# Kernel optimization log

Hardware: AMD Instinct MI355X
Metric: run time of the kernel (lower is better)

The kernel has to match this reference:

```python
import math
import jax, jax.numpy as jnp
import numpy as np

B, T, D = 4, 1024, 1024
H = 16
HD = D // H       # head_dim
DE = 64           # d_event
NT = 8            # n_event_types
NR = 64           # n_rules
NH = 4            # n_hits
NA = 2            # n_alternatives
SQ = math.sqrt(HD)


def setup_inputs() -> dict:
    key = jax.random.key(0)
    ks = jax.random.split(key, 16)
    s = 0.02
    f = jnp.float32
    return {
        "x": jax.random.normal(ks[0], (B, T, D), f),
        "W_node": jax.random.normal(ks[1], (D, D), f) * s,
        "W_value": jax.random.normal(ks[2], (D, D), f) * s,
        "W_out": jax.random.normal(ks[3], (D, D), f) * s,
        "arity_w": jax.random.normal(ks[4], (H, HD), f) * s,   # arity=3 -> one extra axis weight
        "W_event": jax.random.normal(ks[5], (D, DE), f) * s,
        "W_type": jax.random.normal(ks[6], (D, NT), f) * s,
        "patterns": jax.random.normal(ks[7], (NR, DE), f) * s,
        "W_actions": jax.random.normal(ks[8], (NA, D, D), f) * s,
        "W_alt": jax.random.normal(ks[9], (DE, NA), f) * s,
        "log_temp": jnp.zeros((), f),
        "Wg1": jax.random.normal(ks[10], (2 * D + 1, D), f) * s,
        "bg1": jnp.zeros((D,), f),
        "Wg2": jax.random.normal(ks[11], (D, 1), f) * s,
        "bg2": jnp.zeros((1,), f),
    }


def reference(x, W_node, W_value, W_out, arity_w, W_event, W_type, patterns,
              W_actions, W_alt, log_temp, Wg1, bg1, Wg2, bg2):
    # --- IsotropicAttention (arity=3, eval mode so dropout is identity) ---
    nodes = (x @ W_node).reshape(B, T, H, HD).transpose(0, 2, 1, 3)    # (B,H,T,HD)
    values = (x @ W_value).reshape(B, T, H, HD).transpose(0, 2, 1, 3)  # (B,H,T,HD)
    scores = jnp.einsum('bhtd,bhsd->bhts', nodes, nodes)
    scores = (scores + scores.transpose(0, 1, 3, 2)) * (0.5 / SQ)      # symmetrize + scale
    ax = jnp.einsum('bhtd,hd->bht', nodes, arity_w)                    # ternary axis score
    mod = jax.nn.sigmoid((ax[:, :, :, None] + ax[:, :, None, :]) / SQ)
    scores = scores * mod
    attn = jax.nn.softmax(scores, axis=-1)
    attn_out = jnp.einsum('bhts,bhsd->bthd', attn, values).reshape(B, T, D) @ W_out
    x1 = x + attn_out
    # --- EventGenerator ---
    events = x1 @ W_event                                              # (B,T,DE)
    event_types = jax.nn.softmax(x1 @ W_type, axis=-1)                 # (B,T,NT)
    # --- RuleBank: soft top-k hit activation ---
    en = events / jnp.maximum(jnp.linalg.norm(events, axis=-1, keepdims=True), 1e-12)
    pn = patterns / jnp.maximum(jnp.linalg.norm(patterns, axis=-1, keepdims=True), 1e-12)
    sim = en @ pn.T                                                    # (B,T,NR)
    topk_vals, topk_idx = jax.lax.top_k(sim, NH)
    temp = jnp.clip(jnp.exp(log_temp), 0.01, 10.0)
    hit_w = jax.nn.softmax(topk_vals / temp, axis=-1)                  # (B,T,NH)
    hit_patterns = patterns[topk_idx]                                  # (B,T,NH,DE)
    weighted_pattern = jnp.einsum('btkd,btk->btd', hit_patterns, hit_w)
    alt_w = jax.nn.softmax((weighted_pattern @ W_alt) / temp, axis=-1) # (B,T,NA)
    acted = jnp.einsum('btd,ade->btae', x1, W_actions)                 # (B,T,NA,D)
    actions_out = jnp.einsum('btae,bta->bte', acted, alt_w)
    hit_strength = jnp.max(topk_vals, axis=-1, keepdims=True)
    actions_out = actions_out * jax.nn.sigmoid(hit_strength)
    # --- TransactionGate: soft commit/rollback ---
    entropy = -jnp.sum(event_types * jnp.log(event_types + 1e-10), axis=-1, keepdims=True)
    entropy_norm = entropy / math.log(NT)
    gin = jnp.concatenate([x1, actions_out, entropy_norm], axis=-1)    # (B,T,2D+1)
    g = jax.nn.sigmoid(jax.nn.silu(gin @ Wg1 + bg1) @ Wg2 + bg2)       # (B,T,1)
    return x1 + g * actions_out
```

## Files before the change

kernel.cpp:

```cpp
#include <hip/hip_runtime.h>
#include <hip/hip_bf16.h>
#include <math.h>

#define B_  4
#define T_  1024
#define D_  1024
#define H_  16
#define HD_ 64
#define DE_ 64
#define NT_ 8
#define NR_ 64
#define NH_ 4

typedef __attribute__((ext_vector_type(8))) short short8;
typedef __attribute__((ext_vector_type(4))) short short4v;
typedef __attribute__((ext_vector_type(4))) float f4;

__device__ __forceinline__ short f2bf(float f) {
    unsigned x = __float_as_uint(f);
    unsigned r = (x + 0x7fffu + ((x >> 16) & 1u)) >> 16;
    return (short)r;
}
__device__ __forceinline__ float bf2f(short s) {
    return __uint_as_float(((unsigned)(unsigned short)s) << 16);
}

__global__ __launch_bounds__(256) void castx_k(
    const float* __restrict__ x, short* __restrict__ xb)
{
    size_t i = ((size_t)blockIdx.x * 256 + threadIdx.x) * 8;
    float4 v0 = *(const float4*)&x[i];
    float4 v1 = *(const float4*)&x[i + 4];
    short8 o;
    o[0] = f2bf(v0.x); o[1] = f2bf(v0.y); o[2] = f2bf(v0.z); o[3] = f2bf(v0.w);
    o[4] = f2bf(v1.x); o[5] = f2bf(v1.y); o[6] = f2bf(v1.z); o[7] = f2bf(v1.w);
    *(short8*)&xb[i] = o;
}

struct TJ { const float* src; short* dst; int K, N, rs, ro, base; };
struct TJobs { TJ j[7]; };

__global__ __launch_bounds__(256) void tcast_all(TJobs jb)
{
    int bid = blockIdx.x;
    int ji = 0;
#pragma unroll
    for (int i = 1; i < 7; i++) if (bid >= jb.j[i].base) ji = i;
    const float* src = jb.j[ji].src;
    short* dst = jb.j[ji].dst;
    const int K = jb.j[ji].K, N = jb.j[ji].N;
    const int rs = jb.j[ji].rs, ro = jb.j[ji].ro;
    int rel = bid - jb.j[ji].base;
    int tiles_n = N >> 6;
    int k0 = (rel / tiles_n) * 64, n0 = (rel % tiles_n) * 64;

    __shared__ float tile[64][65];
    const int tid = threadIdx.x;
    const int r = tid >> 4, c = (tid & 15) * 4;
#pragma unroll
    for (int rep = 0; rep < 4; rep++) {
        int rr = rep * 16 + r;
        float4 v = *(const float4*)&src[(size_t)(k0 + rr) * N + n0 + c];
        tile[rr][c] = v.x; tile[rr][c + 1] = v.y; tile[rr][c + 2] = v.z; tile[rr][c + 3] = v.w;
    }
    __syncthreads();
#pragma unroll
    for (int rep = 0; rep < 4; rep++) {
        int n = rep * 16 + r;
        short4v p;
        p[0] = f2bf(tile[c + 0][n]);
        p[1] = f2bf(tile[c + 1][n]);
        p[2] = f2bf(tile[c + 2][n]);
        p[3] = f2bf(tile[c + 3][n]);
        *(short4v*)&dst[(size_t)((n0 + n) * rs + ro) * K + k0 + c] = p;
    }
}

__global__ __launch_bounds__(256) void ttype_k(
    const float* __restrict__ Wt, short* __restrict__ BTe)
{
    int idx = blockIdx.x * 256 + threadIdx.x;
    int n = idx >> 10, k = idx & 1023;
    BTe[(size_t)(64 + n) * 1024 + k] = f2bf(Wt[k * 8 + n]);
}

template<int AM>
__global__ __launch_bounds__(256) void gemm4(
    const short* __restrict__ A1, const short* __restrict__ A2, int Ks,
    const short* __restrict__ BT,
    float* __restrict__ C, short* __restrict__ Cb1, short* __restrict__ Cb2,
    int M, int N, int K, int epi,
    const float* __restrict__ resid, const float* __restrict__ ent,
    const float* __restrict__ w1e, const float* __restrict__ bias,
    const float* __restrict__ altw, const float* __restrict__ hitsig)
{
    constexpr int BM = AM * 32;
    constexpr int AR = (AM == 4) ? 2 : 4;
    constexpr int ANV = 64 / AR / 8;
    __shared__ short As[BM * 72];
    __shared__ short Bs[128 * 72];
    const int tid = threadIdx.x, wave = tid >> 6, lane = tid & 63;
    const int lrow = lane & 15, lq = lane >> 4;
    int bid = blockIdx.x;
    int tiles_m = M / BM;
    int mpx = tiles_m >> 3;
    int xcd = bid & 7, idx = bid >> 3;
    int mt = xcd * mpx + (idx % mpx);
    int nt = idx / mpx;
    const int m0 = mt * BM, n0 = nt * 128;
    const int wm = (wave >> 1) * (AM * 16), wn = (wave & 1) * 64;
    const int K2 = K - Ks;
    const int arow = tid / AR, ash = (tid % AR) * (64 / AR);
    const int brow = tid >> 1, bsh = (tid & 1) * 32;

    short8 va[ANV], vb[4];
    auto loadA = [&](int k0) {
        int ka = k0 + ash;
        const short* ap = (ka < Ks)
            ? A1 + (size_t)(m0 + arow) * Ks + ka
            : A2 + (size_t)(m0 + arow) * K2 + (ka - Ks);
#pragma unroll
        for (int u = 0; u < ANV; u++) va[u] = *(const short8*)(ap + u * 8);
    };
    auto loadB = [&](int k0) {
        const short* bp = BT + (size_t)(n0 + brow) * K + k0 + bsh;
#pragma unroll
        for (int u = 0; u < 4; u++) vb[u] = *(const short8*)(bp + u * 8);
    };

    loadA(0); loadB(0);
    f4 acc[AM][4] = {};

    for (int k0 = 0; k0 < K; k0 += 64) {
        __syncthreads();
#pragma unroll
        for (int u = 0; u < ANV; u++)
            *(short8*)&As[arow * 72 + ash + u * 8] = va[u];
#pragma unroll
        for (int u = 0; u < 4; u++)
            *(short8*)&Bs[brow * 72 + bsh + u * 8] = vb[u];
        __syncthreads();
        if (k0 + 64 < K) { loadA(k0 + 64); loadB(k0 + 64); }
#pragma unroll
        for (int kh = 0; kh < 2; kh++) {
            short8 af[AM], bfv[4];
#pragma unroll
            for (int i = 0; i < AM; i++)
                af[i] = *(short8*)&As[(wm + i * 16 + lrow) * 72 + kh * 32 + lq * 8];
#pragma unroll
            for (int j = 0; j < 4; j++)
                bfv[j] = *(short8*)&Bs[(wn + j * 16 + lrow) * 72 + kh * 32 + lq * 8];
#pragma unroll
            for (int i = 0; i < AM; i++)
#pragma unroll
                for (int j = 0; j < 4; j++)
                    acc[i][j] = __builtin_amdgcn_mfma_f32_16x16x32_bf16(
                        af[i], bfv[j], acc[i][j], 0, 0, 0);
        }
    }

#pragma unroll
    for (int i = 0; i < AM; i++) {
#pragma unroll
        for (int r = 0; r < 4; r++) {
            int row = m0 + wm + i * 16 + lq * 4 + r;
            float w0 = 0.f, w1 = 0.f, hs = 0.f;
            if (epi == 5) { w0 = altw[row * 2]; w1 = altw[row * 2 + 1]; hs = hitsig[row]; }
#pragma unroll
            for (int j = 0; j < 4; j++) {
                int col = n0 + wn + j * 16 + lrow;
                float v = acc[i][j][r];
                if (epi == 0) {
                    C[(size_t)row * N + col] = v;
                } else if (epi == 1) {
                    v += resid[(size_t)row * N + col];
                    C[(size_t)row * N + col] = v;
                    Cb1[(size_t)row * N + col] = f2bf(v);
                } else if (epi == 2) {
                    if (col < 1024) Cb1[(size_t)row * 1024 + col] = f2bf(v);
                    else            Cb2[(size_t)row * 1024 + col - 1024] = f2bf(v);
                } else if (epi == 3) {
                    v += ent[row] * w1e[col] + bias[col];
                    float sv = v * __builtin_amdgcn_rcpf(1.f + __expf(-v));
                    Cb1[(size_t)row * N + col] = f2bf(sv);
                } else {
                    float other = __shfl_xor(v, 1);
                    if ((lane & 1) == 0) {
                        float cv = (w0 * v + w1 * other) * hs;
                        Cb1[(size_t)row * 1024 + (col >> 1)] = f2bf(cv);
                    }
                }
            }
        }
    }
}

__global__ __launch_bounds__(256) void vtrans_k(
    const short* __restrict__ vb, short* __restrict__ vtg)
{
    const int b = blockIdx.z, h = blockIdx.y, t0 = blockIdx.x * 64;
    const int tid = threadIdx.x;
    __shared__ short tile[64 * 72];
    const int row = tid >> 2, c = (tid & 3) * 16;
    const short* p = vb + (size_t)(b * T_ + t0 + row) * D_ + h * 64 + c;
    *(short8*)&tile[row * 72 + c + 0] = *(const short8*)(p + 0);
    *(short8*)&tile[row * 72 + c + 8] = *(const short8*)(p + 8);
    __syncthreads();
    short8 o0, o1;
#pragma unroll
    for (int i = 0; i < 8; i++) o0[i] = tile[(c + i) * 72 + row];
#pragma unroll
    for (int i = 0; i < 8; i++) o1[i] = tile[(c + 8 + i) * 72 + row];
    short* q = vtg + (size_t)((b * H_ + h) * 64 + row) * T_ + t0 + c;
    *(short8*)(q + 0) = o0;
    *(short8*)(q + 8) = o1;
}

__global__ __launch_bounds__(256) void ax_k(
    const short* __restrict__ nodes_bf, const float* __restrict__ arity_w,
    float* __restrict__ ax)
{
    int idx = blockIdx.x * 256 + threadIdx.x;
    int t = idx & (T_ - 1);
    int h = (idx >> 10) & (H_ - 1);
    int b = idx >> 14;
    const short* np_ = nodes_bf + (((size_t)b * T_ + t) * H_ + h) * HD_;
    float s = 0.f;
#pragma unroll
    for (int d = 0; d < HD_; d += 8) {
        short8 n8 = *(const short8*)&np_[d];
#pragma unroll
        for (int q = 0; q < 8; q++) s += bf2f(n8[q]) * arity_w[h * HD_ + d + q];
    }
    ax[idx] = s;
}

__global__ __launch_bounds__(256) void attn5_k(
    const short* __restrict__ nodes_bf, const short* __restrict__ vtg,
    const float* __restrict__ ax, short* __restrict__ attnp)
{
    const int b = blockIdx.z, h = blockIdx.y, t0 = blockIdx.x * 64;
    const int tid = threadIdx.x;
    const int wave = tid >> 6, lane = tid & 63;
    const int lrow = lane & 15, lq = lane >> 4;
    const int wm = wave * 16;
    const int row = tid >> 2, c = (tid & 3) * 16;

    __shared__ short Nt[64 * 72];
    __shared__ short Ns[64 * 72];
    __shared__ short Vt[64 * 72];
    __shared__ short Pm[64 * 72];
    __shared__ float axs_sh[64];

    {
        const short* p = nodes_bf + (size_t)(b * T_ + t0 + row) * D_ + h * 64 + c;
        *(short8*)&Nt[row * 72 + c + 0] = *(const short8*)(p + 0);
        *(short8*)&Nt[row * 72 + c + 8] = *(const short8*)(p + 8);
    }
    const float at = ax[(size_t)(b * H_ + h) * T_ + t0 + wm + lrow];
    __syncthreads();
    short8 bt0 = *(short8*)&Nt[(wm + lrow) * 72 + lq * 8];
    short8 bt1 = *(short8*)&Nt[(wm + lrow) * 72 + 32 + lq * 8];

    float l_reg = 0.f;
    f4 O[4] = {};

    for (int s0 = 0; s0 < T_; s0 += 64) {
        __syncthreads();
        {
            const short* p = nodes_bf + (size_t)(b * T_ + s0 + row) * D_ + h * 64 + c;
            *(short8*)&Ns[row * 72 + c + 0] = *(const short8*)(p + 0);
            *(short8*)&Ns[row * 72 + c + 8] = *(const short8*)(p + 8);
            const short* q = vtg + (size_t)((b * H_ + h) * 64 + row) * T_ + s0 + c;
            *(short8*)&Vt[row * 72 + c + 0] = *(const short8*)(q + 0);
            *(short8*)&Vt[row * 72 + c + 8] = *(const short8*)(q + 8);
        }
        if (tid < 64) axs_sh[tid] = ax[(size_t)(b * H_ + h) * T_ + s0 + tid];
        __syncthreads();

        float psum = 0.f;
#pragma unroll
        for (int j = 0; j < 4; j++) {
            short8 a0 = *(short8*)&Ns[(j * 16 + lrow) * 72 + lq * 8];
            short8 a1 = *(short8*)&Ns[(j * 16 + lrow) * 72 + 32 + lq * 8];
            f4 s = {0.f, 0.f, 0.f, 0.f};
            s = __builtin_amdgcn_mfma_f32_16x16x32_bf16(a0, bt0, s, 0, 0, 0);
            s = __builtin_amdgcn_mfma_f32_16x16x32_bf16(a1, bt1, s, 0, 0, 0);
            f4 as4 = *(f4*)&axs_sh[j * 16 + lq * 4];
            short4v pw;
#pragma unroll
            for (int r = 0; r < 4; r++) {
                float z = (at + as4[r]) * 0.125f;
                float mod = 0.5f + z * (0.25f - z * z * 0.020833333f);
                float p = __expf(s[r] * 0.125f * mod);
                psum += p;
                pw[r] = f2bf(p);
            }
            *(short4v*)&Pm[(wm + lrow) * 72 + j * 16 + lq * 4] = pw;
        }
        psum += __shfl_xor(psum, 16);
        psum += __shfl_xor(psum, 32);
        l_reg += psum;

        short8 pa0 = *(short8*)&Pm[(wm + lrow) * 72 + lq * 8];
        short8 pa1 = *(short8*)&Pm[(wm + lrow) * 72 + 32 + lq * 8];
#pragma unroll
        for (int dj = 0; dj < 4; dj++) {
            short8 v0 = *(short8*)&Vt[(dj * 16 + lrow) * 72 + lq * 8];
            short8 v1 = *(short8*)&Vt[(dj * 16 + lrow) * 72 + 32 + lq * 8];
            O[dj] = __builtin_amdgcn_mfma_f32_16x16x32_bf16(pa0, v0, O[dj], 0, 0, 0);
            O[dj] = __builtin_amdgcn_mfma_f32_16x16x32_bf16(pa1, v1, O[dj], 0, 0, 0);
        }
    }

    float linv[4];
#pragma unroll
    for (int r = 0; r < 4; r++)
        linv[r] = __builtin_amdgcn_rcpf(__shfl(l_reg, lq * 4 + r));
#pragma unroll
    for (int dj = 0; dj < 4; dj++)
#pragma unroll
        for (int r = 0; r < 4; r++)
            attnp[(size_t)(b * T_ + t0 + wm + lq * 4 + r) * D_ + h * 64 + dj * 16 + lrow] =
                f2bf(O[dj][r] * linv[r]);
}

__global__ __launch_bounds__(64) void pnorm_k(
    const float* __restrict__ patterns, float* __restrict__ pn)
{
    int r = blockIdx.x, lane = threadIdx.x;
    float v = patterns[r * 64 + lane];
    float ss = v * v;
    for (int off = 1; off < 64; off <<= 1) ss += __shfl_xor(ss, off);
    pn[r * 64 + lane] = v / fmaxf(sqrtf(ss), 1e-12f);
}

__global__ __launch_bounds__(256) void token2_k(
    const float* __restrict__ evlg, const float* __restrict__ pn,
    const float* __restrict__ patterns, const float* __restrict__ W_alt,
    const float* __restrict__ log_temp,
    float* __restrict__ entn, float* __restrict__ altw, float* __restrict__ hitsig)
{
    const int tid = threadIdx.x, wave = tid >> 6, lane = tid & 63;
    __shared__ float pn_sh[64 * 68];
    __shared__ float pat_sh[64 * 68];
    __shared__ float en_sh[4][68];
    {
        int row = tid >> 2, c = (tid & 3) * 16;
#pragma unroll
        for (int u = 0; u < 4; u++) {
            *(float4*)&pn_sh[row * 68 + c + u * 4]  = *(const float4*)&pn[row * 64 + c + u * 4];
            *(float4*)&pat_sh[row * 68 + c + u * 4] = *(const float4*)&patterns[row * 64 + c + u * 4];
        }
    }
    float temp = expf(log_temp[0]);
    temp = fminf(fmaxf(temp, 0.01f), 10.f);
    const float tinv = 1.f / temp;
    __syncthreads();

#pragma unroll
    for (int rep = 0; rep < 2; rep++) {
        const int m = blockIdx.x * 8 + wave * 2 + rep;
        float ev = evlg[(size_t)m * 128 + lane];
        float ss = ev * ev;
        for (int off = 1; off < 64; off <<= 1) ss += __shfl_xor(ss, off);
        float en = ev * __builtin_amdgcn_rcpf(fmaxf(sqrtf(ss), 1e-12f));
        en_sh[wave][lane] = en;
        float entv;
        {
            float lgt = evlg[(size_t)m * 128 + 64 + (lane & 7)];
            float mx = lgt;
            for (int off = 1; off < 8; off <<= 1) mx = fmaxf(mx, __shfl_xor(mx, off));
            float p = __expf(lgt - mx);
            float sum = p;
            for (int off = 1; off < 8; off <<= 1) sum += __shfl_xor(sum, off);
            float pi = p / sum;
            float term = -pi * __logf(pi + 1e-10f);
            float e = term;
            for (int off = 1; off < 8; off <<= 1) e += __shfl_xor(e, off);
            entv = e * 0.4808983f;
        }
        float sim = 0.f;
#pragma unroll
        for (int u = 0; u < 16; u++) {
            float4 e4 = *(float4*)&en_sh[wave][u * 4];
            float4 p4 = *(float4*)&pn_sh[lane * 68 + u * 4];
            sim += e4.x * p4.x + e4.y * p4.y + e4.z * p4.z + e4.w * p4.w;
        }
        float v = sim;
        float tv[NH_]; int tix[NH_];
#pragma unroll
        for (int kk = 0; kk < NH_; kk++) {
            float mv = v; int mi = lane;
            if (v == -1e30f) mi = 127;
            for (int off = 1; off < 64; off <<= 1) {
                float ov = __shfl_xor(mv, off);
                int   oi = __shfl_xor(mi, off);
                if (ov > mv || (ov == mv && oi < mi)) { mv = ov; mi = oi; }
            }
            tv[kk] = mv; tix[kk] = mi;
            if (lane == mi) v = -1e30f;
        }
        float hmx = tv[0];
        float hw[NH_], hsum = 0.f;
#pragma unroll
        for (int kk = 0; kk < NH_; kk++) { hw[kk] = __expf((tv[kk] - hmx) * tinv); hsum += hw[kk]; }
        float hsr = __builtin_amdgcn_rcpf(hsum);
        float wp = 0.f;
#pragma unroll
        for (int kk = 0; kk < NH_; kk++) wp += hw[kk] * hsr * pat_sh[tix[kk] * 68 + lane];
        float a0 = wp * W_alt[lane * 2 + 0];
        float a1 = wp * W_alt[lane * 2 + 1];
        for (int off = 1; off < 64; off <<= 1) {
            a0 += __shfl_xor(a0, off);
            a1 += __shfl_xor(a1, off);
        }
        a0 *= tinv; a1 *= tinv;
        float amx = fmaxf(a0, a1);
        float e0 = __expf(a0 - amx), e1 = __expf(a1 - amx);
        if (lane == 0) {
            float zr = __builtin_amdgcn_rcpf(e0 + e1);
            altw[m * 2 + 0] = e0 * zr;
            altw[m * 2 + 1] = e1 * zr;
            hitsig[m] = __builtin_amdgcn_rcpf(1.f + __expf(-tv[0]));
            entn[m] = entv;
        }
    }
}

__global__ __launch_bounds__(256) void gate_k(
    const short* __restrict__ h1_bf, const float* __restrict__ Wg2,
    const float* __restrict__ bg2, const float* __restrict__ x1,
    const short* __restrict__ actions_bf, float* __restrict__ out)
{
    const int m = blockIdx.x, tid = threadIdx.x;
    float part = 0.f;
    for (int d = tid; d < D_; d += 256)
        part += bf2f(h1_bf[(size_t)m * D_ + d]) * Wg2[d];
    __shared__ float red[256];
    red[tid] = part;
    __syncthreads();
    for (int w = 128; w > 0; w >>= 1) {
        if (tid < w) red[tid] += red[tid + w];
        __syncthreads();
    }
    float g = 1.f / (1.f + expf(-(red[0] + bg2[0])));
    for (int d = tid; d < D_; d += 256) {
        size_t i = (size_t)m * D_ + d;
        out[i] = x1[i] + g * bf2f(actions_bf[i]);
    }
}

extern "C" void kernel_launch(void* const* d_in, const int* in_sizes, int n_in,
                              void* d_out, int out_size, void* d_ws, size_t ws_size,
                              hipStream_t stream)
{
    const float* x        = (const float*)d_in[0];
    const float* W_node   = (const float*)d_in[1];
    const float* W_value  = (const float*)d_in[2];
    const float* W_out    = (const float*)d_in[3];
    const float* arity_w  = (const float*)d_in[4];
    const float* W_event  = (const float*)d_in[5];
    const float* W_type   = (const float*)d_in[6];
    const float* patterns = (const float*)d_in[7];
    const float* W_act    = (const float*)d_in[8];
    const float* W_alt    = (const float*)d_in[9];
    const float* log_temp = (const float*)d_in[10];
    const float* Wg1      = (const float*)d_in[11];
    const float* bg1      = (const float*)d_in[12];
    const float* Wg2      = (const float*)d_in[13];
    const float* bg2      = (const float*)d_in[14];
    float* out = (float*)d_out;

    const int M = B_ * T_;
    float* x1     = (float*)d_ws;
    float* evlg   = x1 + 4194304;
    float* axp    = evlg + 524288;
    float* pn     = axp + 65536;
    float* entn   = pn + 4096;
    float* altw   = entn + 4096;
    float* hitsig = altw + 8192;
    short* big       = (short*)(hitsig + 4096);
    short* xbf       = big;
    short* nodes_bf  = big + 1 * 4194304;
    short* values_bf = big + 2 * 4194304;
    short* vtg       = big + 3 * 4194304;
    short* x1_bf     = big + 4 * 4194304;
    short* wts       = big + 5 * 4194304;
    short* WnvT  = wts;
    short* WoT   = wts + 2 * 1048576;
    short* WaT   = wts + 3 * 1048576;
    short* Wg1T  = wts + 5 * 1048576;
    short* BTe   = wts + 7 * 1048576;
    short* actions_bf = vtg;
    short* h1_bf      = xbf;

    dim3 blk(256);
    dim3 g_bh(T_ / 64, H_, B_);

    castx_k<<<2048, blk, 0, stream>>>(x, xbf);
    pnorm_k<<<NR_, 64, 0, stream>>>(patterns, pn);
    TJobs jb;
    jb.j[0] = {W_node,            WnvT,           1024, 1024, 1, 0,    0};
    jb.j[1] = {W_value,           WnvT + 1048576, 1024, 1024, 1, 0,  256};
    jb.j[2] = {W_out,             WoT,            1024, 1024, 1, 0,  512};
    jb.j[3] = {W_act,             WaT,            1024, 1024, 2, 0,  768};
    jb.j[4] = {W_act + 1048576,   WaT,            1024, 1024, 2, 1, 1024};
    jb.j[5] = {Wg1,               Wg1T,           2048, 1024, 1, 0, 1280};
    jb.j[6] = {W_event,           BTe,            1024,   64, 1, 0, 1792};
    tcast_all<<<1808, blk, 0, stream>>>(jb);
    ttype_k<<<32, blk, 0, stream>>>(W_type, BTe);

    gemm4<4><<<512, blk, 0, stream>>>(xbf, xbf, D_, WnvT,
        nullptr, nodes_bf, values_bf, M, 2048, D_, 2,
        nullptr, nullptr, nullptr, nullptr, nullptr, nullptr);
    ax_k<<<256, blk, 0, stream>>>(nodes_bf, arity_w, axp);
    vtrans_k<<<g_bh, blk, 0, stream>>>(values_bf, vtg);
    attn5_k<<<g_bh, blk, 0, stream>>>(nodes_bf, vtg, axp, xbf);
    gemm4<2><<<512, blk, 0, stream>>>(xbf, xbf, D_, WoT,
        x1, x1_bf, nullptr, M, D_, D_, 1,
        x, nullptr, nullptr, nullptr, nullptr, nullptr);
    gemm4<2><<<64, blk, 0, stream>>>(x1_bf, x1_bf, D_, BTe,
        evlg, nullptr, nullptr, M, 128, D_, 0,
        nullptr, nullptr, nullptr, nullptr, nullptr, nullptr);
    token2_k<<<M / 8, blk, 0, stream>>>(evlg, pn, patterns, W_alt, log_temp,
                                        entn, altw, hitsig);
    gemm4<4><<<512, blk, 0, stream>>>(x1_bf, x1_bf, D_, WaT,
        nullptr, actions_bf, nullptr, M, 2048, D_, 5,
        nullptr, nullptr, nullptr, nullptr, altw, hitsig);
    gemm4<2><<<512, blk, 0, stream>>>(x1_bf, actions_bf, D_, Wg1T,
        nullptr, h1_bf, nullptr, M, D_, 2048, 3,
        nullptr, entn, Wg1 + (size_t)2048 * D_, bg1, nullptr, nullptr);
    gate_k<<<M, blk, 0, stream>>>(h1_bf, Wg2, bg2, x1, actions_bf, out);
}
```

Before: 347.8 us.

## Register-prefetch next attention tile and streamline softmax exponent arithmetic

The attention kernel now loads the next key/value/axis tile into registers while computing the current tile, so global-load latency overlaps the MFMA work. It also reads the query fragments straight from global memory instead of staging them in shared memory. The sigmoid-polynomial and exp are folded into exp2 with pre-scaled constants, the bf16 pack uses the hardware packed-convert instruction, and the row-sum shuffle reduction moves out of the loop to run once at the end. This raises register pressure and adds small numeric differences from the folded constants.

```diff
diff --git a/kernel.cpp b/kernel.cpp
--- a/kernel.cpp
+++ b/kernel.cpp
@@ -14,6 +14,7 @@
 
 typedef __attribute__((ext_vector_type(8))) short short8;
 typedef __attribute__((ext_vector_type(4))) short short4v;
+typedef __attribute__((ext_vector_type(2))) unsigned uint2v;
 typedef __attribute__((ext_vector_type(4))) float f4;
 
 __device__ __forceinline__ short f2bf(float f) {
@@ -235,7 +236,7 @@
     ax[idx] = s;
 }
 
-__global__ __launch_bounds__(256) void attn5_k(
+__global__ __launch_bounds__(256) void attn6_k(
     const short* __restrict__ nodes_bf, const short* __restrict__ vtg,
     const float* __restrict__ ax, short* __restrict__ attnp)
 {
@@ -246,37 +247,47 @@
     const int wm = wave * 16;
     const int row = tid >> 2, c = (tid & 3) * 16;
 
-    __shared__ short Nt[64 * 72];
     __shared__ short Ns[64 * 72];
     __shared__ short Vt[64 * 72];
     __shared__ short Pm[64 * 72];
     __shared__ float axs_sh[64];
 
-    {
-        const short* p = nodes_bf + (size_t)(b * T_ + t0 + row) * D_ + h * 64 + c;
-        *(short8*)&Nt[row * 72 + c + 0] = *(const short8*)(p + 0);
-        *(short8*)&Nt[row * 72 + c + 8] = *(const short8*)(p + 8);
-    }
-    const float at = ax[(size_t)(b * H_ + h) * T_ + t0 + wm + lrow];
-    __syncthreads();
-    short8 bt0 = *(short8*)&Nt[(wm + lrow) * 72 + lq * 8];
-    short8 bt1 = *(short8*)&Nt[(wm + lrow) * 72 + 32 + lq * 8];
+    const short* qp = nodes_bf + (size_t)(b * T_ + t0 + wm + lrow) * D_ + h * 64;
+    const short8 bt0 = *(const short8*)(qp + lq * 8);
+    const short8 bt1 = *(const short8*)(qp + 32 + lq * 8);
+    const float at8 = ax[(size_t)(b * H_ + h) * T_ + t0 + wm + lrow] * 0.125f;
+
+    const short* np0 = nodes_bf + (size_t)(b * T_ + row) * D_ + h * 64 + c;
+    const short* vp0 = vtg + (size_t)((b * H_ + h) * 64 + row) * T_ + c;
+    const float* axp_ = ax + (size_t)(b * H_ + h) * T_;
+
+    short8 vn0 = *(const short8*)(np0 + 0);
+    short8 vn1 = *(const short8*)(np0 + 8);
+    short8 vv0 = *(const short8*)(vp0 + 0);
+    short8 vv1 = *(const short8*)(vp0 + 8);
+    float axv = 0.f;
+    if (tid < 64) axv = axp_[tid] * 0.125f;
 
     float l_reg = 0.f;
     f4 O[4] = {};
 
     for (int s0 = 0; s0 < T_; s0 += 64) {
         __syncthreads();
-        {
-            const short* p = nodes_bf + (size_t)(b * T_ + s0 + row) * D_ + h * 64 + c;
-            *(short8*)&Ns[row * 72 + c + 0] = *(const short8*)(p + 0);
-            *(short8*)&Ns[row * 72 + c + 8] = *(const short8*)(p + 8);
-            const short* q = vtg + (size_t)((b * H_ + h) * 64 + row) * T_ + s0 + c;
-            *(short8*)&Vt[row * 72 + c + 0] = *(const short8*)(q + 0);
-            *(short8*)&Vt[row * 72 + c + 8] = *(const short8*)(q + 8);
-        }
-        if (tid < 64) axs_sh[tid] = ax[(size_t)(b * H_ + h) * T_ + s0 + tid];
+        *(short8*)&Ns[row * 72 + c + 0] = vn0;
+        *(short8*)&Ns[row * 72 + c + 8] = vn1;
+        *(short8*)&Vt[row * 72 + c + 0] = vv0;
+        *(short8*)&Vt[row * 72 + c + 8] = vv1;
+        if (tid < 64) axs_sh[tid] = axv;
         __syncthreads();
+        if (s0 + 64 < T_) {
+            const short* np = np0 + (size_t)(s0 + 64) * D_;
+            const short* vp = vp0 + (s0 + 64);
+            vn0 = *(const short8*)(np + 0);
+            vn1 = *(const short8*)(np + 8);
+            vv0 = *(const short8*)(vp + 0);
+            vv1 = *(const short8*)(vp + 8);
+            if (tid < 64) axv = axp_[s0 + 64 + tid] * 0.125f;
+        }
 
         float psum = 0.f;
 #pragma unroll
@@ -287,19 +298,33 @@
             s = __builtin_amdgcn_mfma_f32_16x16x32_bf16(a0, bt0, s, 0, 0, 0);
             s = __builtin_amdgcn_mfma_f32_16x16x32_bf16(a1, bt1, s, 0, 0, 0);
             f4 as4 = *(f4*)&axs_sh[j * 16 + lq * 4];
-            short4v pw;
-#pragma unroll
-            for (int r = 0; r < 4; r++) {
-                float z = (at + as4[r]) * 0.125f;
-                float mod = 0.5f + z * (0.25f - z * z * 0.020833333f);
-                float p = __expf(s[r] * 0.125f * mod);
-                psum += p;
-                pw[r] = f2bf(p);
+            float p0, p1, p2, p3;
+            {
+                float z, zz, t1, mK;
+                z = at8 + as4[0]; zz = z * z;
+                t1 = fmaf(zz, -0.0037570183f, 0.04508422f);
+                mK = fmaf(z, t1, 0.09016844f);
+                p0 = __builtin_amdgcn_exp2f(s[0] * mK);
+                z = at8 + as4[1]; zz = z * z;
+                t1 = fmaf(zz, -0.0037570183f, 0.04508422f);
+                mK = fmaf(z, t1, 0.09016844f);
+                p1 = __builtin_amdgcn_exp2f(s[1] * mK);
+                z = at8 + as4[2]; zz = z * z;
+                t1 = fmaf(zz, -0.0037570183f, 0.04508422f);
+                mK = fmaf(z, t1, 0.09016844f);
+                p2 = __builtin_amdgcn_exp2f(s[2] * mK);
+                z = at8 + as4[3]; zz = z * z;
+                t1 = fmaf(zz, -0.0037570183f, 0.04508422f);
+                mK = fmaf(z, t1, 0.09016844f);
+                p3 = __builtin_amdgcn_exp2f(s[3] * mK);
             }
-            *(short4v*)&Pm[(wm + lrow) * 72 + j * 16 + lq * 4] = pw;
-        }
-        psum += __shfl_xor(psum, 16);
-        psum += __shfl_xor(psum, 32);
+            psum += (p0 + p1) + (p2 + p3);
+            unsigned u0, u1;
+            asm("v_cvt_pk_bf16_f32 %0, %1, %2" : "=v"(u0) : "v"(p0), "v"(p1));
+            asm("v_cvt_pk_bf16_f32 %0, %1, %2" : "=v"(u1) : "v"(p2), "v"(p3));
+            uint2v uu; uu[0] = u0; uu[1] = u1;
+            *(uint2v*)&Pm[(wm + lrow) * 72 + j * 16 + lq * 4] = uu;
+        }
         l_reg += psum;
 
         short8 pa0 = *(short8*)&Pm[(wm + lrow) * 72 + lq * 8];
@@ -312,6 +337,9 @@
             O[dj] = __builtin_amdgcn_mfma_f32_16x16x32_bf16(pa1, v1, O[dj], 0, 0, 0);
         }
     }
+
+    l_reg += __shfl_xor(l_reg, 16);
+    l_reg += __shfl_xor(l_reg, 32);
 
     float linv[4];
 #pragma unroll
@@ -516,7 +544,7 @@
         nullptr, nullptr, nullptr, nullptr, nullptr, nullptr);
     ax_k<<<256, blk, 0, stream>>>(nodes_bf, arity_w, axp);
     vtrans_k<<<g_bh, blk, 0, stream>>>(values_bf, vtg);
-    attn5_k<<<g_bh, blk, 0, stream>>>(nodes_bf, vtg, axp, xbf);
+    attn6_k<<<g_bh, blk, 0, stream>>>(nodes_bf, vtg, axp, xbf);
     gemm4<2><<<512, blk, 0, stream>>>(xbf, xbf, D_, WoT,
         x1, x1_bf, nullptr, M, D_, D_, 1,
         x, nullptr, nullptr, nullptr, nullptr, nullptr);
```

Result: no change. 342.4 us (-1.6%).
